# Kernel tuning notes

Measured on AMD Instinct MI355X. Metric: run time of the kernel, lower is better.

Reference implementation:

```python
import jax, jax.numpy as jnp
import numpy as np

N_NODES = 100000
N_EDGE_PAIRS = 800000  # undirected pairs -> 1.6M directed edges
DIM_IN = 128
NUM_CLASSES = 16
N_ITERS = 5


def _log_normalize(a):
    return a - jax.nn.logsumexp(a, axis=-1, keepdims=True)


def setup_inputs() -> dict:
    key = jax.random.key(0)
    k1, k2, k3, k4, k5 = jax.random.split(key, 5)
    # reciprocal directed edges: edges 2i and 2i+1 are reverses of each other
    src = jax.random.randint(k1, (N_EDGE_PAIRS,), 0, N_NODES)
    dst = jax.random.randint(k2, (N_EDGE_PAIRS,), 0, N_NODES)
    e_src = jnp.stack([src, dst], axis=1).reshape(-1)  # [E]
    e_dst = jnp.stack([dst, src], axis=1).reshape(-1)  # [E]
    edge_index = jnp.stack([e_src, e_dst], axis=0)     # [2, E]
    E = e_src.shape[0]
    rv = jnp.arange(E).reshape(-1, 2)[:, ::-1].reshape(-1)  # reverse-edge permutation
    x = jax.random.normal(k3, (N_NODES, DIM_IN), dtype=jnp.float32)
    W = jax.random.normal(k4, (DIM_IN, NUM_CLASSES), dtype=jnp.float32) * 0.1
    b = jnp.zeros((NUM_CLASSES,), dtype=jnp.float32)
    dim_param = NUM_CLASSES * (NUM_CLASSES + 1) // 2
    param = jax.random.normal(k5, (dim_param,), dtype=jnp.float32) * 0.1
    return {"x": x, "W": W, "b": b, "param": param,
            "edge_index": edge_index, "rv": rv}


def reference(x, W, b, param, edge_index, rv):
    N = x.shape[0]
    C = W.shape[1]
    # MLP (num_hidden=0 -> single Linear) + LogSoftmax
    log_b0 = jax.nn.log_softmax(x @ W + b, axis=-1)  # [N, C]
    # coupling matrix logH (symmetric), detached since learn_coupling=False
    rid, cid = np.tril_indices(C)
    logT = jnp.zeros((C, C), dtype=x.dtype).at[rid, cid].set(
        jax.nn.log_sigmoid(param * 10.0))
    logH = logT + jnp.triu(logT.T, 1)
    logH = jax.lax.stop_gradient(logH)
    src, dst = edge_index[0], edge_index[1]
    E = src.shape[0]
    log_msg = jnp.full((E, C), -float(np.log(C)), dtype=x.dtype)
    log_b = log_b0
    for _ in range(N_ITERS):
        # message: gather beliefs at source, subtract reverse message
        t = log_b[src] - log_msg[rv]                                    # [E, C]
        raw = jax.nn.logsumexp(t[:, :, None] + logH[None, :, :], axis=1)  # [E, C]
        log_msg = _log_normalize(raw)
        # aggregate (scatter-add) into destination nodes, then update
        agg = jax.ops.segment_sum(log_msg, dst, num_segments=N)         # [N, C]
        log_b = _log_normalize(agg + log_b0)
    return log_b
```

## Files before the change

### kernel.cpp

```cpp
#include <hip/hip_runtime.h>
#include <math.h>

#define NN      100000
#define EE      1600000
#define NPAIRS  800000
#define DIN     128
#define CC      16
#define NITERS  5
#define PPT     4
#define NGRP    (NPAIRS / PPT)
#define NEGLOGC (-2.772588722239781f)

typedef float  f4 __attribute__((ext_vector_type(4)));
typedef int    i2 __attribute__((ext_vector_type(2)));

__device__ __forceinline__ unsigned short f2bf(float f) {
    unsigned int u = __float_as_uint(f);
    unsigned int r = u + 0x7fffu + ((u >> 16) & 1u);
    return (unsigned short)(r >> 16);
}
__device__ __forceinline__ unsigned int pack_bf(float lo, float hi) {
    return (unsigned int)f2bf(lo) | ((unsigned int)f2bf(hi) << 16);
}

__global__ __launch_bounds__(256) void k_setup(
    const float* __restrict__ x, const float* __restrict__ W,
    const float* __restrict__ b, const float* __restrict__ param,
    float* __restrict__ M, float* __restrict__ logb0, float* __restrict__ agg)
{
    if (blockIdx.x == 0 && threadIdx.x < CC * (CC + 1) / 2) {
        int i = threadIdx.x;
        int r = 0;
        while ((r + 1) * (r + 2) / 2 <= i) ++r;
        int c = i - r * (r + 1) / 2;
        float z = param[i] * 10.0f;
        float s = 1.0f / (1.0f + __expf(-z));
        M[r * CC + c] = s;
        if (r != c) M[c * CC + r] = s;
    }

    int idx  = blockIdx.x * 256 + threadIdx.x;
    agg[idx] = 0.f;

    int node = idx >> 4;
    int cls  = idx & 15;
    const f4* xr4 = (const f4*)(x + (long)node * DIN);
    float acc = b[cls];
#pragma unroll 8
    for (int k4 = 0; k4 < DIN / 4; ++k4) {
        f4 xv = __builtin_nontemporal_load(xr4 + k4);
        acc = fmaf(xv.x, W[(4 * k4 + 0) * CC + cls], acc);
        acc = fmaf(xv.y, W[(4 * k4 + 1) * CC + cls], acc);
        acc = fmaf(xv.z, W[(4 * k4 + 2) * CC + cls], acc);
        acc = fmaf(xv.w, W[(4 * k4 + 3) * CC + cls], acc);
    }
    float m = acc;
    for (int off = 8; off; off >>= 1) m = fmaxf(m, __shfl_xor(m, off, 16));
    float s = __expf(acc - m);
    for (int off = 8; off; off >>= 1) s += __shfl_xor(s, off, 16);
    logb0[idx] = acc - m - __logf(s);
}

template <bool RD_MSG, bool WR_MSG>
__global__ __launch_bounds__(256) void k_edges_t(
    const i2* __restrict__ esrc2, const i2* __restrict__ edst2,
    const float* __restrict__ logb, const float* __restrict__ Mg,
    unsigned int* __restrict__ msg2, float* __restrict__ agg)
{
    __shared__ float sM[CC * CC];
    __shared__ float sE[PPT][16 * 40];
    sM[threadIdx.x] = Mg[threadIdx.x];
    __syncthreads();

    const int lane = threadIdx.x & 15;
    const int gl   = threadIdx.x >> 4;
    const int g    = blockIdx.x * 16 + gl;

    float Hrow[CC];
#pragma unroll
    for (int k = 0; k < CC; ++k) Hrow[k] = sM[k * CC + lane];

    i2 s01[PPT], d01[PPT];
    unsigned int mold[PPT];
#pragma unroll
    for (int r = 0; r < PPT; ++r) {
        int p = g + r * NGRP;
        s01[r] = __builtin_nontemporal_load(esrc2 + p);
        d01[r] = __builtin_nontemporal_load(edst2 + p);
        if (RD_MSG)
            mold[r] = __builtin_nontemporal_load(msg2 + (long)p * CC + lane);
    }

#pragma unroll
    for (int r = 0; r < PPT; ++r) {
        float lb0 = logb[(long)s01[r].x * CC + lane];
        float lb1 = logb[(long)s01[r].y * CC + lane];
        float mo0, mo1;
        if (RD_MSG) {
            mo0 = __uint_as_float(mold[r] << 16);
            mo1 = __uint_as_float(mold[r] & 0xffff0000u);
        } else {
            mo0 = NEGLOGC; mo1 = NEGLOGC;
        }
        float* eb = sE[r] + gl * 40;
        eb[lane]      = __expf(lb0 - mo1);
        eb[16 + lane] = __expf(lb1 - mo0);
    }

#pragma unroll
    for (int r = 0; r < PPT; ++r) {
        const float* eb = sE[r] + gl * 40;
        float ev0[CC], ev1[CC];
        *(float4*)(ev0 +  0) = *(const float4*)(eb +  0);
        *(float4*)(ev0 +  4) = *(const float4*)(eb +  4);
        *(float4*)(ev0 +  8) = *(const float4*)(eb +  8);
        *(float4*)(ev0 + 12) = *(const float4*)(eb + 12);
        *(float4*)(ev1 +  0) = *(const float4*)(eb + 16);
        *(float4*)(ev1 +  4) = *(const float4*)(eb + 20);
        *(float4*)(ev1 +  8) = *(const float4*)(eb + 24);
        *(float4*)(ev1 + 12) = *(const float4*)(eb + 28);

        float S0 = 0.f, S1 = 0.f;
#pragma unroll
        for (int k = 0; k < CC; ++k) {
            S0 = fmaf(ev0[k], Hrow[k], S0);
            S1 = fmaf(ev1[k], Hrow[k], S1);
        }

        float T0 = S0, T1 = S1;
        for (int off = 8; off; off >>= 1) {
            T0 += __shfl_xor(T0, off, 16);
            T1 += __shfl_xor(T1, off, 16);
        }
        float n0 = __logf(S0) - __logf(T0);
        float n1 = __logf(S1) - __logf(T1);

        if (WR_MSG) {
            int p = g + r * NGRP;
            __builtin_nontemporal_store(pack_bf(n0, n1),
                                        msg2 + (long)p * CC + lane);
        }
        atomicAdd(&agg[(long)d01[r].x * CC + lane], n0);
        atomicAdd(&agg[(long)d01[r].y * CC + lane], n1);
    }
}

__global__ __launch_bounds__(256) void k_update(
    const float* __restrict__ logb0, float* __restrict__ agg,
    float* __restrict__ out)
{
    int idx = blockIdx.x * blockDim.x + threadIdx.x;
    float v = agg[idx] + logb0[idx];
    agg[idx] = 0.f;
    float m = v;
    for (int off = 8; off; off >>= 1) m = fmaxf(m, __shfl_xor(m, off, 16));
    float s = __expf(v - m);
    for (int off = 8; off; off >>= 1) s += __shfl_xor(s, off, 16);
    out[idx] = v - m - __logf(s);
}

extern "C" void kernel_launch(void* const* d_in, const int* in_sizes, int n_in,
                              void* d_out, int out_size, void* d_ws, size_t ws_size,
                              hipStream_t stream)
{
    const float* x     = (const float*)d_in[0];
    const float* W     = (const float*)d_in[1];
    const float* b     = (const float*)d_in[2];
    const float* param = (const float*)d_in[3];
    const int*   eidx  = (const int*)d_in[4];
    const i2*    esrc2 = (const i2*)eidx;
    const i2*    edst2 = (const i2*)(eidx + EE);

    float* ws    = (float*)d_ws;
    float* M     = ws;
    float* logb0 = M     + 256;
    float* logb  = logb0 + (long)NN * CC;
    float* agg   = logb  + (long)NN * CC;
    unsigned int* msg2 = (unsigned int*)(agg + (long)NN * CC);

    k_setup<<<NN * CC / 256, 256, 0, stream>>>(x, W, b, param, M, logb0, agg);

    const float* curb = logb0;
    for (int it = 0; it < NITERS; ++it) {
        if (it == 0)
            k_edges_t<false, true><<<NGRP / 16, 256, 0, stream>>>(
                esrc2, edst2, curb, M, msg2, agg);
        else if (it == NITERS - 1)
            k_edges_t<true, false><<<NGRP / 16, 256, 0, stream>>>(
                esrc2, edst2, curb, M, msg2, agg);
        else
            k_edges_t<true, true><<<NGRP / 16, 256, 0, stream>>>(
                esrc2, edst2, curb, M, msg2, agg);
        float* dst = (it == NITERS - 1) ? (float*)d_out : logb;
        k_update<<<NN * CC / 256, 256, 0, stream>>>(logb0, agg, dst);
        curb = dst;
    }
}
```

Baseline: 612.8 us.

## Replace atomic scatter-add aggregation with CSR-based gather over destination nodes

Builds a CSR index of incoming edges per destination node (degree count, multi-level prefix scan, cursor scatter) once at setup. The edge kernel now only writes bf16 messages, and a new per-node kernel gathers and sums the incoming messages before applying the log-normalize update. This removes the 1.6M float atomics per iteration and the zeroing of agg. The cost is several extra setup kernels, a random gather of message rows in the aggregation, and an edge order inside each node set by atomics, so float summation order is nondeterministic.

```diff
diff --git a/kernel.cpp b/kernel.cpp
--- a/kernel.cpp
+++ b/kernel.cpp
@@ -9,6 +9,7 @@
 #define NITERS  5
 #define PPT     4
 #define NGRP    (NPAIRS / PPT)
+#define NBLK    ((NN + 255) / 256)
 #define NEGLOGC (-2.772588722239781f)
 
 typedef float  f4 __attribute__((ext_vector_type(4)));
@@ -19,14 +20,16 @@
     unsigned int r = u + 0x7fffu + ((u >> 16) & 1u);
     return (unsigned short)(r >> 16);
 }
-__device__ __forceinline__ unsigned int pack_bf(float lo, float hi) {
-    return (unsigned int)f2bf(lo) | ((unsigned int)f2bf(hi) << 16);
+__device__ __forceinline__ float bf2f(unsigned short u) {
+    return __uint_as_float((unsigned int)u << 16);
 }
 
 __global__ __launch_bounds__(256) void k_setup(
     const float* __restrict__ x, const float* __restrict__ W,
     const float* __restrict__ b, const float* __restrict__ param,
-    float* __restrict__ M, float* __restrict__ logb0, float* __restrict__ agg)
+    const int* __restrict__ edst,
+    float* __restrict__ M, float* __restrict__ logb0,
+    unsigned int* __restrict__ deg)
 {
     if (blockIdx.x == 0 && threadIdx.x < CC * (CC + 1) / 2) {
         int i = threadIdx.x;
@@ -39,8 +42,9 @@
         if (r != c) M[c * CC + r] = s;
     }
 
-    int idx  = blockIdx.x * 256 + threadIdx.x;
-    agg[idx] = 0.f;
+    int idx = blockIdx.x * 256 + threadIdx.x;
+
+    atomicAdd(&deg[edst[idx]], 1u);
 
     int node = idx >> 4;
     int cls  = idx & 15;
@@ -61,11 +65,68 @@
     logb0[idx] = acc - m - __logf(s);
 }
 
-template <bool RD_MSG, bool WR_MSG>
+__global__ __launch_bounds__(256) void k_scan_blk(
+    const unsigned int* __restrict__ deg, unsigned int* __restrict__ rowtmp,
+    unsigned int* __restrict__ bsum)
+{
+    __shared__ unsigned int s[256];
+    int t = threadIdx.x, i = blockIdx.x * 256 + t;
+    unsigned int v = (i < NN) ? deg[i] : 0u;
+    s[t] = v; __syncthreads();
+    for (int off = 1; off < 256; off <<= 1) {
+        unsigned int a = (t >= off) ? s[t - off] : 0u;
+        __syncthreads();
+        s[t] += a;
+        __syncthreads();
+    }
+    if (i < NN) rowtmp[i] = s[t] - v;
+    if (t == 255) bsum[blockIdx.x] = s[255];
+}
+
+__global__ __launch_bounds__(512) void k_scan_top(
+    const unsigned int* __restrict__ bsum, unsigned int* __restrict__ boff)
+{
+    __shared__ unsigned int s[512];
+    int t = threadIdx.x;
+    unsigned int v = (t < NBLK) ? bsum[t] : 0u;
+    s[t] = v; __syncthreads();
+    for (int off = 1; off < 512; off <<= 1) {
+        unsigned int a = (t >= off) ? s[t - off] : 0u;
+        __syncthreads();
+        s[t] += a;
+        __syncthreads();
+    }
+    boff[t] = s[t] - v;
+}
+
+__global__ __launch_bounds__(256) void k_scan_add(
+    const unsigned int* __restrict__ rowtmp, const unsigned int* __restrict__ boff,
+    unsigned int* __restrict__ row, unsigned int* __restrict__ cursor)
+{
+    int i = blockIdx.x * 256 + threadIdx.x;
+    if (i < NN) {
+        unsigned int r = rowtmp[i] + boff[blockIdx.x];
+        row[i]    = r;
+        cursor[i] = r;
+    }
+    if (i == 0) row[NN] = EE;
+}
+
+__global__ __launch_bounds__(256) void k_csrscat(
+    const int* __restrict__ edst, unsigned int* __restrict__ cursor,
+    unsigned int* __restrict__ csr)
+{
+    int e = blockIdx.x * 256 + threadIdx.x;
+    int d = edst[e];
+    unsigned int pos = atomicAdd(&cursor[d], 1u);
+    csr[pos] = (unsigned int)e;
+}
+
+template <bool RD_MSG>
 __global__ __launch_bounds__(256) void k_edges_t(
-    const i2* __restrict__ esrc2, const i2* __restrict__ edst2,
+    const i2* __restrict__ esrc2,
     const float* __restrict__ logb, const float* __restrict__ Mg,
-    unsigned int* __restrict__ msg2, float* __restrict__ agg)
+    unsigned short* __restrict__ msg)
 {
     __shared__ float sM[CC * CC];
     __shared__ float sE[PPT][16 * 40];
@@ -80,28 +141,24 @@
 #pragma unroll
     for (int k = 0; k < CC; ++k) Hrow[k] = sM[k * CC + lane];
 
-    i2 s01[PPT], d01[PPT];
-    unsigned int mold[PPT];
+    i2 s01[PPT];
+    unsigned short m0[PPT], m1[PPT];
 #pragma unroll
     for (int r = 0; r < PPT; ++r) {
         int p = g + r * NGRP;
         s01[r] = __builtin_nontemporal_load(esrc2 + p);
-        d01[r] = __builtin_nontemporal_load(edst2 + p);
-        if (RD_MSG)
-            mold[r] = __builtin_nontemporal_load(msg2 + (long)p * CC + lane);
+        if (RD_MSG) {
+            m0[r] = __builtin_nontemporal_load(msg + (long)(2 * p)     * CC + lane);
+            m1[r] = __builtin_nontemporal_load(msg + (long)(2 * p + 1) * CC + lane);
+        }
     }
 
 #pragma unroll
     for (int r = 0; r < PPT; ++r) {
         float lb0 = logb[(long)s01[r].x * CC + lane];
         float lb1 = logb[(long)s01[r].y * CC + lane];
-        float mo0, mo1;
-        if (RD_MSG) {
-            mo0 = __uint_as_float(mold[r] << 16);
-            mo1 = __uint_as_float(mold[r] & 0xffff0000u);
-        } else {
-            mo0 = NEGLOGC; mo1 = NEGLOGC;
-        }
+        float mo0 = RD_MSG ? bf2f(m0[r]) : NEGLOGC;
+        float mo1 = RD_MSG ? bf2f(m1[r]) : NEGLOGC;
         float* eb = sE[r] + gl * 40;
         eb[lane]      = __expf(lb0 - mo1);
         eb[16 + lane] = __expf(lb1 - mo0);
@@ -135,23 +192,41 @@
         float n0 = __logf(S0) - __logf(T0);
         float n1 = __logf(S1) - __logf(T1);
 
-        if (WR_MSG) {
-            int p = g + r * NGRP;
-            __builtin_nontemporal_store(pack_bf(n0, n1),
-                                        msg2 + (long)p * CC + lane);
-        }
-        atomicAdd(&agg[(long)d01[r].x * CC + lane], n0);
-        atomicAdd(&agg[(long)d01[r].y * CC + lane], n1);
-    }
-}
-
-__global__ __launch_bounds__(256) void k_update(
-    const float* __restrict__ logb0, float* __restrict__ agg,
+        int p = g + r * NGRP;
+        __builtin_nontemporal_store(f2bf(n0), msg + (long)(2 * p)     * CC + lane);
+        __builtin_nontemporal_store(f2bf(n1), msg + (long)(2 * p + 1) * CC + lane);
+    }
+}
+
+__global__ __launch_bounds__(256) void k_agg(
+    const unsigned int* __restrict__ row, const unsigned int* __restrict__ csr,
+    const unsigned short* __restrict__ msg, const float* __restrict__ logb0,
     float* __restrict__ out)
 {
-    int idx = blockIdx.x * blockDim.x + threadIdx.x;
-    float v = agg[idx] + logb0[idx];
-    agg[idx] = 0.f;
+    int idx = blockIdx.x * 256 + threadIdx.x;
+    int n = idx >> 4, c = idx & 15;
+    unsigned int beg = row[n], end = row[n + 1];
+
+    float acc = 0.f;
+    unsigned int base = beg;
+    for (; base + 16 <= end; base += 16) {
+        int eid = (int)csr[base + c];
+#pragma unroll
+        for (int j = 0; j < 16; ++j) {
+            int e = __shfl(eid, j, 16);
+            acc += bf2f(msg[(long)e * CC + c]);
+        }
+    }
+    if (base < end) {
+        int cnt = (int)(end - base);
+        int eid = (base + c < end) ? (int)csr[base + c] : 0;
+        for (int j = 0; j < cnt; ++j) {
+            int e = __shfl(eid, j, 16);
+            acc += bf2f(msg[(long)e * CC + c]);
+        }
+    }
+
+    float v = acc + logb0[idx];
     float m = v;
     for (int off = 8; off; off >>= 1) m = fmaxf(m, __shfl_xor(m, off, 16));
     float s = __expf(v - m);
@@ -169,30 +244,36 @@
     const float* param = (const float*)d_in[3];
     const int*   eidx  = (const int*)d_in[4];
     const i2*    esrc2 = (const i2*)eidx;
-    const i2*    edst2 = (const i2*)(eidx + EE);
-
-    float* ws    = (float*)d_ws;
-    float* M     = ws;
-    float* logb0 = M     + 256;
-    float* logb  = logb0 + (long)NN * CC;
-    float* agg   = logb  + (long)NN * CC;
-    unsigned int* msg2 = (unsigned int*)(agg + (long)NN * CC);
-
-    k_setup<<<NN * CC / 256, 256, 0, stream>>>(x, W, b, param, M, logb0, agg);
+    const int*   edst  = eidx + EE;
+
+    char* w = (char*)d_ws;
+    float*          M      = (float*)w;          w += 256 * 4;
+    float*          logb0  = (float*)w;          w += (long)NN * CC * 4;
+    float*          logb   = (float*)w;          w += (long)NN * CC * 4;
+    unsigned int*   deg    = (unsigned int*)w;   w += (long)NN * 4;
+    unsigned int*   rowtmp = (unsigned int*)w;   w += (long)NN * 4;
+    unsigned int*   bsum   = (unsigned int*)w;   w += 512 * 4;
+    unsigned int*   boff   = (unsigned int*)w;   w += 512 * 4;
+    unsigned int*   rowp   = (unsigned int*)w;   w += (long)(NN + 16) * 4;
+    unsigned int*   cursor = (unsigned int*)w;   w += (long)NN * 4;
+    unsigned int*   csr    = (unsigned int*)w;   w += (long)EE * 4;
+    unsigned short* msg    = (unsigned short*)w;
+
+    hipMemsetAsync(deg, 0, (long)NN * 4, stream);
+    k_setup   <<<NN * CC / 256, 256, 0, stream>>>(x, W, b, param, edst, M, logb0, deg);
+    k_scan_blk<<<NBLK, 256, 0, stream>>>(deg, rowtmp, bsum);
+    k_scan_top<<<1, 512, 0, stream>>>(bsum, boff);
+    k_scan_add<<<NBLK, 256, 0, stream>>>(rowtmp, boff, rowp, cursor);
+    k_csrscat <<<EE / 256, 256, 0, stream>>>(edst, cursor, csr);
 
     const float* curb = logb0;
     for (int it = 0; it < NITERS; ++it) {
         if (it == 0)
-            k_edges_t<false, true><<<NGRP / 16, 256, 0, stream>>>(
-                esrc2, edst2, curb, M, msg2, agg);
-        else if (it == NITERS - 1)
-            k_edges_t<true, false><<<NGRP / 16, 256, 0, stream>>>(
-                esrc2, edst2, curb, M, msg2, agg);
+            k_edges_t<false><<<NGRP / 16, 256, 0, stream>>>(esrc2, curb, M, msg);
         else
-            k_edges_t<true, true><<<NGRP / 16, 256, 0, stream>>>(
-                esrc2, edst2, curb, M, msg2, agg);
+            k_edges_t<true><<<NGRP / 16, 256, 0, stream>>>(esrc2, curb, M, msg);
         float* dst = (it == NITERS - 1) ? (float*)d_out : logb;
-        k_update<<<NN * CC / 256, 256, 0, stream>>>(logb0, agg, dst);
+        k_agg<<<NN * CC / 256, 256, 0, stream>>>(rowp, csr, msg, logb0, dst);
         curb = dst;
     }
 }
```

Result: slower. 779.2 us (+27.2%).

## Accumulate edge messages as packed fixed-point integers via 64-bit atomics

Applied to the files above, without the earlier changes.

Replaces float atomicAdd scatter into node aggregates with unsigned fixed-point (2^20 scale) accumulation of negated log-messages, packing two adjacent classes into one 64-bit integer atomic. This halves the number of atomic operations and uses integer atomics, which may be cheaper than float atomics on this hardware. It relies on messages being non-positive and on no carry crossing the 32-bit halves; very negative messages or high-degree nodes could overflow a lane and corrupt the neighbouring class, and quantization adds error.

```diff
diff --git a/kernel.cpp b/kernel.cpp
--- a/kernel.cpp
+++ b/kernel.cpp
@@ -10,9 +10,12 @@
 #define PPT     4
 #define NGRP    (NPAIRS / PPT)
 #define NEGLOGC (-2.772588722239781f)
+#define FPSCALE 1048576.0f
+#define FPINV   (1.0f / 1048576.0f)
 
 typedef float  f4 __attribute__((ext_vector_type(4)));
 typedef int    i2 __attribute__((ext_vector_type(2)));
+typedef unsigned long long ull;
 
 __device__ __forceinline__ unsigned short f2bf(float f) {
     unsigned int u = __float_as_uint(f);
@@ -26,7 +29,8 @@
 __global__ __launch_bounds__(256) void k_setup(
     const float* __restrict__ x, const float* __restrict__ W,
     const float* __restrict__ b, const float* __restrict__ param,
-    float* __restrict__ M, float* __restrict__ logb0, float* __restrict__ agg)
+    float* __restrict__ M, float* __restrict__ logb0,
+    unsigned int* __restrict__ agg32)
 {
     if (blockIdx.x == 0 && threadIdx.x < CC * (CC + 1) / 2) {
         int i = threadIdx.x;
@@ -39,8 +43,8 @@
         if (r != c) M[c * CC + r] = s;
     }
 
-    int idx  = blockIdx.x * 256 + threadIdx.x;
-    agg[idx] = 0.f;
+    int idx = blockIdx.x * 256 + threadIdx.x;
+    agg32[idx] = 0u;
 
     int node = idx >> 4;
     int cls  = idx & 15;
@@ -65,7 +69,7 @@
 __global__ __launch_bounds__(256) void k_edges_t(
     const i2* __restrict__ esrc2, const i2* __restrict__ edst2,
     const float* __restrict__ logb, const float* __restrict__ Mg,
-    unsigned int* __restrict__ msg2, float* __restrict__ agg)
+    unsigned int* __restrict__ msg2, ull* __restrict__ agg8)
 {
     __shared__ float sM[CC * CC];
     __shared__ float sE[PPT][16 * 40];
@@ -140,18 +144,27 @@
             __builtin_nontemporal_store(pack_bf(n0, n1),
                                         msg2 + (long)p * CC + lane);
         }
-        atomicAdd(&agg[(long)d01[r].x * CC + lane], n0);
-        atomicAdd(&agg[(long)d01[r].y * CC + lane], n1);
+
+        unsigned int q0 = (unsigned int)(fmaxf(-n0, 0.f) * FPSCALE + 0.5f);
+        unsigned int q1 = (unsigned int)(fmaxf(-n1, 0.f) * FPSCALE + 0.5f);
+        unsigned int p0 = __shfl_xor(q0, 1, 16);
+        unsigned int p1 = __shfl_xor(q1, 1, 16);
+        bool odd = lane & 1;
+        ull  val  = odd ? ((ull)p1 | ((ull)q1 << 32))
+                        : ((ull)q0 | ((ull)p0 << 32));
+        int  node = odd ? d01[r].y : d01[r].x;
+        atomicAdd(&agg8[(long)node * 8 + (lane >> 1)], val);
     }
 }
 
 __global__ __launch_bounds__(256) void k_update(
-    const float* __restrict__ logb0, float* __restrict__ agg,
+    const float* __restrict__ logb0, unsigned int* __restrict__ agg32,
     float* __restrict__ out)
 {
     int idx = blockIdx.x * blockDim.x + threadIdx.x;
-    float v = agg[idx] + logb0[idx];
-    agg[idx] = 0.f;
+    unsigned int q = agg32[idx];
+    agg32[idx] = 0u;
+    float v = fmaf(-(float)q, FPINV, logb0[idx]);
     float m = v;
     for (int off = 8; off; off >>= 1) m = fmaxf(m, __shfl_xor(m, off, 16));
     float s = __expf(v - m);
@@ -175,24 +188,25 @@
     float* M     = ws;
     float* logb0 = M     + 256;
     float* logb  = logb0 + (long)NN * CC;
-    float* agg   = logb  + (long)NN * CC;
-    unsigned int* msg2 = (unsigned int*)(agg + (long)NN * CC);
-
-    k_setup<<<NN * CC / 256, 256, 0, stream>>>(x, W, b, param, M, logb0, agg);
+    unsigned int* agg32 = (unsigned int*)(logb + (long)NN * CC);
+    ull*          agg8  = (ull*)agg32;
+    unsigned int* msg2  = agg32 + (long)NN * CC;
+
+    k_setup<<<NN * CC / 256, 256, 0, stream>>>(x, W, b, param, M, logb0, agg32);
 
     const float* curb = logb0;
     for (int it = 0; it < NITERS; ++it) {
         if (it == 0)
             k_edges_t<false, true><<<NGRP / 16, 256, 0, stream>>>(
-                esrc2, edst2, curb, M, msg2, agg);
+                esrc2, edst2, curb, M, msg2, agg8);
         else if (it == NITERS - 1)
             k_edges_t<true, false><<<NGRP / 16, 256, 0, stream>>>(
-                esrc2, edst2, curb, M, msg2, agg);
+                esrc2, edst2, curb, M, msg2, agg8);
         else
             k_edges_t<true, true><<<NGRP / 16, 256, 0, stream>>>(
-                esrc2, edst2, curb, M, msg2, agg);
+                esrc2, edst2, curb, M, msg2, agg8);
         float* dst = (it == NITERS - 1) ? (float*)d_out : logb;
-        k_update<<<NN * CC / 256, 256, 0, stream>>>(logb0, agg, dst);
+        k_update<<<NN * CC / 256, 256, 0, stream>>>(logb0, agg32, dst);
         curb = dst;
     }
 }
```

Measured after the change: 576.9 us. -5.9%, faster.
